# Kernel optimization log

Measured on AMD Instinct MI355X. Metric: run time of the kernel, lower is better.

The kernel has to match this reference:

```python
import jax, jax.numpy as jnp
import numpy as np

E = 20    # number of residue types (rc.restypes)
NB = 2    # num_blocks per AngleHead
NA = 7    # num_angles
C_S = 384
C_H = 128
BS, L = 8, 2048


def setup_inputs() -> dict:
    key = jax.random.key(0)
    ks = jax.random.split(key, 16)
    sc = 0.02
    return {
        "s": jax.random.normal(ks[0], (BS, L, C_S), dtype=jnp.float32),
        "s_init": jax.random.normal(ks[1], (BS, L, C_S), dtype=jnp.float32),
        "aatype": jax.random.randint(ks[2], (BS, L), 0, E, dtype=jnp.int32),
        # stacked per-residue-type AngleHead params
        "Win": jax.random.normal(ks[3], (E, C_S, C_H), dtype=jnp.float32) * sc,
        "b_in": jax.random.normal(ks[4], (E, C_H), dtype=jnp.float32) * sc,
        "Winit": jax.random.normal(ks[5], (E, C_S, C_H), dtype=jnp.float32) * sc,
        "b_init2": jax.random.normal(ks[6], (E, C_H), dtype=jnp.float32) * sc,
        "Wb1": jax.random.normal(ks[7], (E, NB, C_H, C_H), dtype=jnp.float32) * sc,
        "bb1": jax.random.normal(ks[8], (E, NB, C_H), dtype=jnp.float32) * sc,
        "Wb2": jax.random.normal(ks[9], (E, NB, C_H, C_H), dtype=jnp.float32) * sc,
        "bb2": jax.random.normal(ks[10], (E, NB, C_H), dtype=jnp.float32) * sc,
        "Wout": jax.random.normal(ks[11], (E, C_H, NA * 2), dtype=jnp.float32) * sc,
        "b_out": jax.random.normal(ks[12], (E, NA * 2), dtype=jnp.float32) * sc,
    }


def reference(s, s_init, aatype, Win, b_in, Winit, b_init2, Wb1, bb1, Wb2, bb2, Wout, b_out):
    relu = jax.nn.relu
    bs, seq_len, c_s = s.shape
    N = bs * seq_len
    sf = s.reshape(N, c_s)          # [N, c_s]
    si = s_init.reshape(N, c_s)     # [N, c_s]

    # Dense dispatch: run every token through all E per-type heads, then
    # combine with the one-hot routing mask (math identical to the torch
    # gather/scatter loop over residue types).
    h = jnp.einsum('nd,edh->neh', relu(sf), Win) + b_in            # [N,E,H]
    h = h + jnp.einsum('nd,edh->neh', relu(si), Winit) + b_init2   # [N,E,H]

    for b in range(NB):  # ResidualBlock1d: s + W2 @ relu(W1 @ relu(s))
        a = jnp.einsum('neh,ehk->nek', relu(h), Wb1[:, b]) + bb1[:, b]
        a = jnp.einsum('nek,ekh->neh', relu(a), Wb2[:, b]) + bb2[:, b]
        h = h + a

    out = jnp.einsum('neh,eho->neo', relu(h), Wout) + b_out        # [N,E,2*NA]
    sel = jax.nn.one_hot(aatype.reshape(N), E, dtype=out.dtype)    # [N,E]
    ang = jnp.einsum('neo,ne->no', out, sel).reshape(bs, seq_len, NA, 2)

    # F.normalize(dim=-1): x / max(||x||, eps)
    nrm = jnp.maximum(jnp.linalg.norm(ang, axis=-1, keepdims=True), 1e-12)
    return ang / nrm
```

## Files before the change

### kernel.cpp

```cpp
#include <hip/hip_runtime.h>
#include <math.h>

#define E_TYPES 20
#define NBLK 2
#define NANG 7
#define CS 384
#define CH 128
#define N_TOK (8 * 2048)
#define TOK 32
#define TPB 256
#define PREPB 256
#define GRID_M 536
#define PADN 2048

#define CNT_OFF 0
#define PERM_OFF 64
#define WT1_OFF (256 * 1024)
#define WT1_SZ  (20 * 8 * 24 * 2048)
#define WTR_OFF (WT1_OFF + WT1_SZ)

typedef __attribute__((ext_vector_type(8))) short bfrag;
typedef __attribute__((ext_vector_type(4))) float f32x4;

__device__ __forceinline__ void split_bf16(float x, unsigned short& h, unsigned short& l) {
    unsigned int u = __float_as_uint(x);
    unsigned int hb = (u + 0x7FFFu + ((u >> 16) & 1u)) & 0xFFFF0000u;
    h = (unsigned short)(hb >> 16);
    float r = x - __uint_as_float(hb);
    unsigned int v = __float_as_uint(r);
    l = (unsigned short)((v + 0x7FFFu + ((v >> 16) & 1u)) >> 16);
}

__global__ __launch_bounds__(PREPB)
void prep_k(const float* __restrict__ Win, const float* __restrict__ Winit,
            const float* __restrict__ Wb1, const float* __restrict__ Wb2,
            const int* __restrict__ aatype, int* __restrict__ wsI,
            unsigned short* __restrict__ wt)
{
    __shared__ unsigned short tp[4][2][32][134];
    __shared__ int lh[E_TYPES], lcur[E_TYPES];
    int bid = blockIdx.x, t = threadIdx.x;

    if (bid < 64) {
        if (t < E_TYPES) { lh[t] = 0; lcur[t] = 0; }
        __syncthreads();
        for (int i = t; i < bid * 256; i += 256) atomicAdd(&lh[aatype[i]], 1);
        __syncthreads();
        int idx = bid * 256 + t;
        int e = aatype[idx];
        int r = lh[e] + atomicAdd(&lcur[e], 1);
        if (r < PADN) wsI[PERM_OFF + e * PADN + r] = idx;
        if (bid == 63) {
            __syncthreads();
            if (t < E_TYPES) wsI[CNT_OFF + t] = lh[t] + lcur[t];
        }
        return;
    }

    int w = t >> 6, lane = t & 63, lane15 = lane & 15, quad = lane >> 4;
    int wid = (bid - 64) * 4 + w;
    const float* srcbase;
    int phase1, e, kt, m4 = 0;
    if (wid < 480) {
        phase1 = 1;
        e = wid / 24; kt = wid % 24;
        srcbase = (kt < 12) ? Win   + ((size_t)e * CS + kt * 32) * CH
                            : Winit + ((size_t)e * CS + (kt - 12) * 32) * CH;
    } else {
        phase1 = 0;
        int rid = wid - 480;
        e = rid >> 4; m4 = (rid >> 2) & 3; kt = rid & 3;
        const float* W = (m4 & 1) ? Wb2 : Wb1;
        srcbase = W + (((size_t)e * NBLK + (m4 >> 1)) * CH + kt * 32) * CH;
    }

    #pragma unroll 4
    for (int i = 0; i < 16; i++) {
        int idx = i * 64 + lane;
        int row = idx >> 5, c4 = idx & 31;
        float4 v = *(const float4*)(srcbase + (size_t)row * CH + c4 * 4);
        ushort4 hv, lv;
        split_bf16(v.x, hv.x, lv.x);
        split_bf16(v.y, hv.y, lv.y);
        split_bf16(v.z, hv.z, lv.z);
        split_bf16(v.w, hv.w, lv.w);
        *(ushort4*)&tp[w][0][row][c4 * 4] = hv;
        *(ushort4*)&tp[w][1][row][c4 * 4] = lv;
    }
    #pragma unroll
    for (int nt = 0; nt < 8; nt++) {
        bfrag hb, lb;
        #pragma unroll
        for (int j = 0; j < 8; j++) {
            hb[j] = (short)tp[w][0][quad * 8 + j][nt * 16 + lane15];
            lb[j] = (short)tp[w][1][quad * 8 + j][nt * 16 + lane15];
        }
        size_t blk = phase1 ? (size_t)((e * 8 + nt) * 24 + kt)
                            : (size_t)((((e * 4 + m4) * 8) + nt) * 4 + kt);
        unsigned short* dst = wt + (phase1 ? WT1_OFF / 2 : WTR_OFF / 2)
                              + blk * 1024 + lane * 8;
        *(bfrag*)dst = hb;
        *(bfrag*)(dst + 512) = lb;
    }
}

#define MFMA(a, b, c) __builtin_amdgcn_mfma_f32_16x16x32_bf16((a), (b), (c), 0, 0, 0)

#define KSTEP(AH0, AL0, AH1, AL1, B, ACC)                    \
    ACC[0][0] = MFMA(AH0, B[0], ACC[0][0]);                  \
    ACC[0][0] = MFMA(AH0, B[1], ACC[0][0]);                  \
    ACC[0][0] = MFMA(AL0, B[0], ACC[0][0]);                  \
    ACC[0][1] = MFMA(AH0, B[2], ACC[0][1]);                  \
    ACC[0][1] = MFMA(AH0, B[3], ACC[0][1]);                  \
    ACC[0][1] = MFMA(AL0, B[2], ACC[0][1]);                  \
    ACC[1][0] = MFMA(AH1, B[0], ACC[1][0]);                  \
    ACC[1][0] = MFMA(AH1, B[1], ACC[1][0]);                  \
    ACC[1][0] = MFMA(AL1, B[0], ACC[1][0]);                  \
    ACC[1][1] = MFMA(AH1, B[2], ACC[1][1]);                  \
    ACC[1][1] = MFMA(AH1, B[3], ACC[1][1]);                  \
    ACC[1][1] = MFMA(AL1, B[2], ACC[1][1]);

__global__ __launch_bounds__(TPB)
void angle_main(const float* __restrict__ s, const float* __restrict__ si,
                const float* __restrict__ b_in, const float* __restrict__ b_init2,
                const float* __restrict__ bb1, const float* __restrict__ bb2,
                const float* __restrict__ Wout, const float* __restrict__ b_out,
                const int* __restrict__ wsI, const unsigned short* __restrict__ wt,
                float* __restrict__ out)
{
    __shared__ __align__(16) unsigned char smem_raw[32768];
    typedef unsigned short AfragT[2][2][512][8];
    AfragT& Afrag = *reinterpret_cast<AfragT*>(smem_raw);
    float (*Hf)[132] = reinterpret_cast<float(*)[132]>(smem_raw);
    float (*Of)[16]  = reinterpret_cast<float(*)[16]>(smem_raw + 16896);
    __shared__ int ptok[TOK];
    __shared__ int poffs[E_TYPES + 1];

    int t = threadIdx.x;
    if (t <= E_TYPES) {
        int off = 0;
        for (int e = 0; e < t; e++)
            off += (wsI[CNT_OFF + e] + TOK - 1) & ~(TOK - 1);
        poffs[t] = off;
    }
    __syncthreads();

    int bid = blockIdx.x;
    int tile = (bid & 7) * (GRID_M / 8) + (bid >> 3);
    int pos = tile * TOK;
    if (pos >= poffs[E_TYPES]) return;
    int e = 0;
    while (e < E_TYPES - 1 && pos >= poffs[e + 1]) e++;
    int n = wsI[CNT_OFF + e] - (pos - poffs[e]);
    if (n > TOK) n = TOK;
    if (t < TOK)
        ptok[t] = wsI[PERM_OFF + e * PADN + (pos - poffs[e]) + ((t < n) ? t : 0)];

    int w = t >> 6, lane = t & 63, lane15 = lane & 15, quad = lane >> 4;
    int nc0 = (2 * w) * 16 + lane15, nc1 = nc0 + 16;

    __syncthreads();

    const bfrag* wt1 = (const bfrag*)((const char*)wt + WT1_OFF);
    const bfrag* wtr = (const bfrag*)((const char*)wt + WTR_OFF);

    f32x4 acc[2][2];
    {
        float bv0 = b_in[e * CH + nc0] + b_init2[e * CH + nc0];
        float bv1 = b_in[e * CH + nc1] + b_init2[e * CH + nc1];
        #pragma unroll
        for (int mt = 0; mt < 2; mt++) {
            acc[mt][0] = (f32x4){bv0, bv0, bv0, bv0};
            acc[mt][1] = (f32x4){bv1, bv1, bv1, bv1};
        }
    }

    int stok = t >> 3, sc = t & 7;
    const float* rowp_s  = s  + (size_t)ptok[stok] * CS;
    const float* rowp_si = si + (size_t)ptok[stok] * CS;

    float4 pf[2][4];
    #pragma unroll
    for (int q = 0; q < 4; q++)
        pf[0][q] = *(const float4*)(rowp_s + sc * 4 + 32 * q);

    bfrag Bc[4], Bn[4];

    #pragma unroll
    for (int c = 0; c < 6; c++) {
        int buf = c & 1;
        __syncthreads();
        #pragma unroll
        for (int q = 0; q < 4; q++) {
            float4 v = pf[buf][q];
            ushort4 hv, lv;
            split_bf16(fmaxf(v.x, 0.f), hv.x, lv.x);
            split_bf16(fmaxf(v.y, 0.f), hv.y, lv.y);
            split_bf16(fmaxf(v.z, 0.f), hv.z, lv.z);
            split_bf16(fmaxf(v.w, 0.f), hv.w, lv.w);
            int fi = (q * 4 + (sc >> 1)) * 32 + stok;
            *(ushort4*)&Afrag[buf][0][fi][(sc & 1) * 4] = hv;
            *(ushort4*)&Afrag[buf][1][fi][(sc & 1) * 4] = lv;
        }
        __syncthreads();
        if (c + 1 < 6) {
            const float* rp = ((c + 1) < 3 ? rowp_s : rowp_si) + ((c + 1) % 3) * 128;
            #pragma unroll
            for (int q = 0; q < 4; q++)
                pf[(c + 1) & 1][q] = *(const float4*)(rp + sc * 4 + 32 * q);
        }
        {
            size_t b0 = ((size_t)(e * 8 + 2 * w) * 24 + c * 4) * 128;
            size_t b1 = ((size_t)(e * 8 + 2 * w + 1) * 24 + c * 4) * 128;
            Bc[0] = wt1[b0 + lane]; Bc[1] = wt1[b0 + 64 + lane];
            Bc[2] = wt1[b1 + lane]; Bc[3] = wt1[b1 + 64 + lane];
        }
        #pragma unroll
        for (int ks = 0; ks < 4; ks++) {
            if (ks < 3) {
                int kb = c * 4 + ks + 1;
                size_t b0 = ((size_t)(e * 8 + 2 * w) * 24 + kb) * 128;
                size_t b1 = ((size_t)(e * 8 + 2 * w + 1) * 24 + kb) * 128;
                Bn[0] = wt1[b0 + lane]; Bn[1] = wt1[b0 + 64 + lane];
                Bn[2] = wt1[b1 + lane]; Bn[3] = wt1[b1 + 64 + lane];
            }
            int fib = (ks * 4 + quad) * 32;
            bfrag ah0 = *(const bfrag*)&Afrag[buf][0][fib + lane15][0];
            bfrag ah1 = *(const bfrag*)&Afrag[buf][0][fib + 16 + lane15][0];
            bfrag al0 = *(const bfrag*)&Afrag[buf][1][fib + lane15][0];
            bfrag al1 = *(const bfrag*)&Afrag[buf][1][fib + 16 + lane15][0];
            KSTEP(ah0, al0, ah1, al1, Bc, acc)
            #pragma unroll
            for (int z = 0; z < 4; z++) Bc[z] = Bn[z];
        }
    }

    f32x4 a2[2][2];
    #pragma unroll
    for (int b = 0; b < NBLK; b++) {
        #pragma unroll
        for (int stage = 0; stage < 2; stage++) {
            int g = 2 * b + stage;
            __syncthreads();
            #pragma unroll
            for (int mt = 0; mt < 2; mt++)
                #pragma unroll
                for (int nl = 0; nl < 2; nl++) {
                    f32x4 v = (stage == 0) ? acc[mt][nl] : a2[mt][nl];
                    int nn = (2 * w + nl) * 16 + lane15;
                    int fib = ((nn >> 5) * 4 + ((nn >> 3) & 3)) * 32;
                    int j = nn & 7;
                    #pragma unroll
                    for (int r = 0; r < 4; r++) {
                        int m = mt * 16 + quad * 4 + r;
                        unsigned short hh, ll;
                        split_bf16(fmaxf(v[r], 0.f), hh, ll);
                        Afrag[0][0][fib + m][j] = hh;
                        Afrag[0][1][fib + m][j] = ll;
                    }
                }
            __syncthreads();

            const float* bias = (stage == 0) ? bb1 : bb2;
            f32x4 an[2][2];
            {
                float bv0 = bias[(e * NBLK + b) * CH + nc0];
                float bv1 = bias[(e * NBLK + b) * CH + nc1];
                #pragma unroll
                for (int mt = 0; mt < 2; mt++) {
                    an[mt][0] = (f32x4){bv0, bv0, bv0, bv0};
                    an[mt][1] = (f32x4){bv1, bv1, bv1, bv1};
                }
            }
            {
                size_t b0 = ((size_t)((e * 4 + g) * 8 + 2 * w) * 4) * 128;
                size_t b1 = ((size_t)((e * 4 + g) * 8 + 2 * w + 1) * 4) * 128;
                Bc[0] = wtr[b0 + lane]; Bc[1] = wtr[b0 + 64 + lane];
                Bc[2] = wtr[b1 + lane]; Bc[3] = wtr[b1 + 64 + lane];
            }
            #pragma unroll
            for (int ks = 0; ks < 4; ks++) {
                if (ks < 3) {
                    size_t b0 = ((size_t)((e * 4 + g) * 8 + 2 * w) * 4 + ks + 1) * 128;
                    size_t b1 = ((size_t)((e * 4 + g) * 8 + 2 * w + 1) * 4 + ks + 1) * 128;
                    Bn[0] = wtr[b0 + lane]; Bn[1] = wtr[b0 + 64 + lane];
                    Bn[2] = wtr[b1 + lane]; Bn[3] = wtr[b1 + 64 + lane];
                }
                int fib = (ks * 4 + quad) * 32;
                bfrag ah0 = *(const bfrag*)&Afrag[0][0][fib + lane15][0];
                bfrag ah1 = *(const bfrag*)&Afrag[0][0][fib + 16 + lane15][0];
                bfrag al0 = *(const bfrag*)&Afrag[0][1][fib + lane15][0];
                bfrag al1 = *(const bfrag*)&Afrag[0][1][fib + 16 + lane15][0];
                KSTEP(ah0, al0, ah1, al1, Bc, an)
                #pragma unroll
                for (int z = 0; z < 4; z++) Bc[z] = Bn[z];
            }
            if (stage == 0) {
                #pragma unroll
                for (int mt = 0; mt < 2; mt++)
                    #pragma unroll
                    for (int nl = 0; nl < 2; nl++) a2[mt][nl] = an[mt][nl];
            } else {
                #pragma unroll
                for (int mt = 0; mt < 2; mt++)
                    #pragma unroll
                    for (int nl = 0; nl < 2; nl++) acc[mt][nl] += an[mt][nl];
            }
        }
    }

    __syncthreads();
    #pragma unroll
    for (int mt = 0; mt < 2; mt++)
        #pragma unroll
        for (int nl = 0; nl < 2; nl++) {
            f32x4 v = acc[mt][nl];
            int nn = (2 * w + nl) * 16 + lane15;
            #pragma unroll
            for (int r = 0; r < 4; r++)
                Hf[mt * 16 + quad * 4 + r][nn] = fmaxf(v[r], 0.f);
        }
    __syncthreads();

    const float* WoutE = Wout + (size_t)e * CH * (NANG * 2);
    const float* boutE = b_out + (size_t)e * (NANG * 2);
    for (int idx = t; idx < n * (NANG * 2); idx += TPB) {
        int i = idx / (NANG * 2);
        int o = idx % (NANG * 2);
        float v = boutE[o];
        #pragma unroll 4
        for (int k = 0; k < CH; k++)
            v = fmaf(Hf[i][k], WoutE[(size_t)k * (NANG * 2) + o], v);
        Of[i][o] = v;
    }
    __syncthreads();

    for (int idx = t; idx < n * NANG; idx += TPB) {
        int i = idx / NANG;
        int a = idx % NANG;
        float x = Of[i][2 * a];
        float y = Of[i][2 * a + 1];
        float nr = fmaxf(sqrtf(x * x + y * y), 1e-12f);
        size_t base = (size_t)ptok[i] * (NANG * 2) + 2 * a;
        out[base]     = x / nr;
        out[base + 1] = y / nr;
    }
}

extern "C" void kernel_launch(void* const* d_in, const int* in_sizes, int n_in,
                              void* d_out, int out_size, void* d_ws, size_t ws_size,
                              hipStream_t stream) {
    const float* s       = (const float*)d_in[0];
    const float* s_init  = (const float*)d_in[1];
    const int*   aatype  = (const int*)d_in[2];
    const float* Win     = (const float*)d_in[3];
    const float* b_in    = (const float*)d_in[4];
    const float* Winit   = (const float*)d_in[5];
    const float* b_init2 = (const float*)d_in[6];
    const float* Wb1     = (const float*)d_in[7];
    const float* bb1     = (const float*)d_in[8];
    const float* Wb2     = (const float*)d_in[9];
    const float* bb2     = (const float*)d_in[10];
    const float* Wout    = (const float*)d_in[11];
    const float* b_out   = (const float*)d_in[12];
    int* wsI = (int*)d_ws;
    unsigned short* wt = (unsigned short*)d_ws;
    float* out = (float*)d_out;

    hipLaunchKernelGGL(prep_k, dim3(64 + 200), dim3(PREPB), 0, stream,
                       Win, Winit, Wb1, Wb2, aatype, wsI, wt);
    hipLaunchKernelGGL(angle_main, dim3(GRID_M), dim3(TPB), 0, stream,
                       s, s_init, b_in, b_init2, bb1, bb2, Wout, b_out,
                       wsI, wt, out);
}
```

Before: 168.2 us.

## Stage weight fragments into LDS via global_load_lds and swizzle A tiles

Weight B fragments are now copied from global memory straight into per-wave LDS buffers with global_load_lds (16-byte DMA) instead of being loaded into registers with software double buffering. The A fragment tile is shrunk to 64-wide K chunks (12 steps instead of 6), and an XOR swizzle is applied to its LDS layout to cut bank conflicts. The aim is to lower VGPR pressure and global-load latency stalls. In exchange the kernel uses more LDS per block (48KB), which can reduce occupancy, and it synchronises more often per K chunk.

```diff
diff --git a/kernel.cpp b/kernel.cpp
--- a/kernel.cpp
+++ b/kernel.cpp
@@ -21,6 +21,13 @@
 
 typedef __attribute__((ext_vector_type(8))) short bfrag;
 typedef __attribute__((ext_vector_type(4))) float f32x4;
+typedef unsigned int u32;
+typedef __attribute__((address_space(1))) const u32 gu32;
+typedef __attribute__((address_space(3))) u32 lu32;
+
+__device__ __forceinline__ void dma16(const void* g, void* l) {
+    __builtin_amdgcn_global_load_lds((gu32*)g, (lu32*)l, 16, 0, 0);
+}
 
 __device__ __forceinline__ void split_bf16(float x, unsigned short& h, unsigned short& l) {
     unsigned int u = __float_as_uint(x);
@@ -29,6 +36,10 @@
     float r = x - __uint_as_float(hb);
     unsigned int v = __float_as_uint(r);
     l = (unsigned short)((v + 0x7FFFu + ((v >> 16) & 1u)) >> 16);
+}
+
+__device__ __forceinline__ int SWZ(int K, int m) {
+    return K * 32 + (m ^ ((4 * K) & 31));
 }
 
 __global__ __launch_bounds__(PREPB)
@@ -106,19 +117,21 @@
 
 #define MFMA(a, b, c) __builtin_amdgcn_mfma_f32_16x16x32_bf16((a), (b), (c), 0, 0, 0)
 
-#define KSTEP(AH0, AL0, AH1, AL1, B, ACC)                    \
-    ACC[0][0] = MFMA(AH0, B[0], ACC[0][0]);                  \
-    ACC[0][0] = MFMA(AH0, B[1], ACC[0][0]);                  \
-    ACC[0][0] = MFMA(AL0, B[0], ACC[0][0]);                  \
-    ACC[0][1] = MFMA(AH0, B[2], ACC[0][1]);                  \
-    ACC[0][1] = MFMA(AH0, B[3], ACC[0][1]);                  \
-    ACC[0][1] = MFMA(AL0, B[2], ACC[0][1]);                  \
-    ACC[1][0] = MFMA(AH1, B[0], ACC[1][0]);                  \
-    ACC[1][0] = MFMA(AH1, B[1], ACC[1][0]);                  \
-    ACC[1][0] = MFMA(AL1, B[0], ACC[1][0]);                  \
-    ACC[1][1] = MFMA(AH1, B[2], ACC[1][1]);                  \
-    ACC[1][1] = MFMA(AH1, B[3], ACC[1][1]);                  \
-    ACC[1][1] = MFMA(AL1, B[2], ACC[1][1]);
+#define KSTEP(AH0, AL0, AH1, AL1, BH0, BL0, BH1, BL1, ACC)   \
+    ACC[0][0] = MFMA(AH0, BH0, ACC[0][0]);                   \
+    ACC[0][0] = MFMA(AH0, BL0, ACC[0][0]);                   \
+    ACC[0][0] = MFMA(AL0, BH0, ACC[0][0]);                   \
+    ACC[0][1] = MFMA(AH0, BH1, ACC[0][1]);                   \
+    ACC[0][1] = MFMA(AH0, BL1, ACC[0][1]);                   \
+    ACC[0][1] = MFMA(AL0, BH1, ACC[0][1]);                   \
+    ACC[1][0] = MFMA(AH1, BH0, ACC[1][0]);                   \
+    ACC[1][0] = MFMA(AH1, BL0, ACC[1][0]);                   \
+    ACC[1][0] = MFMA(AL1, BH0, ACC[1][0]);                   \
+    ACC[1][1] = MFMA(AH1, BH1, ACC[1][1]);                   \
+    ACC[1][1] = MFMA(AH1, BL1, ACC[1][1]);                   \
+    ACC[1][1] = MFMA(AL1, BH1, ACC[1][1]);
+
+#define AIDX(buf, p, fi) ((((buf) * 2 + (p)) * 256 + (fi)) * 8)
 
 __global__ __launch_bounds__(TPB)
 void angle_main(const float* __restrict__ s, const float* __restrict__ si,
@@ -128,11 +141,11 @@
                 const int* __restrict__ wsI, const unsigned short* __restrict__ wt,
                 float* __restrict__ out)
 {
-    __shared__ __align__(16) unsigned char smem_raw[32768];
-    typedef unsigned short AfragT[2][2][512][8];
-    AfragT& Afrag = *reinterpret_cast<AfragT*>(smem_raw);
-    float (*Hf)[132] = reinterpret_cast<float(*)[132]>(smem_raw);
-    float (*Of)[16]  = reinterpret_cast<float(*)[16]>(smem_raw + 16896);
+    __shared__ __align__(16) unsigned char smem_raw[49152];
+    unsigned short* A = (unsigned short*)smem_raw;
+    unsigned char*  Bb = smem_raw + 16384;
+    float (*Hf)[132] = reinterpret_cast<float(*)[132]>(smem_raw + 16384);
+    float (*Of)[16]  = reinterpret_cast<float(*)[16]>(smem_raw + 16384 + 16896);
     __shared__ int ptok[TOK];
     __shared__ int poffs[E_TYPES + 1];
 
@@ -158,11 +171,9 @@
 
     int w = t >> 6, lane = t & 63, lane15 = lane & 15, quad = lane >> 4;
     int nc0 = (2 * w) * 16 + lane15, nc1 = nc0 + 16;
+    unsigned char* Bw = Bb + w * 8192;
 
     __syncthreads();
-
-    const bfrag* wt1 = (const bfrag*)((const char*)wt + WT1_OFF);
-    const bfrag* wtr = (const bfrag*)((const char*)wt + WTR_OFF);
 
     f32x4 acc[2][2];
     {
@@ -178,60 +189,56 @@
     int stok = t >> 3, sc = t & 7;
     const float* rowp_s  = s  + (size_t)ptok[stok] * CS;
     const float* rowp_si = si + (size_t)ptok[stok] * CS;
-
-    float4 pf[2][4];
-    #pragma unroll
-    for (int q = 0; q < 4; q++)
-        pf[0][q] = *(const float4*)(rowp_s + sc * 4 + 32 * q);
-
-    bfrag Bc[4], Bn[4];
-
-    #pragma unroll
-    for (int c = 0; c < 6; c++) {
+    int fiA = SWZ(sc, stok);
+
+    float4 pf[2][2];
+    pf[0][0] = *(const float4*)(rowp_s + sc * 8);
+    pf[0][1] = *(const float4*)(rowp_s + sc * 8 + 4);
+
+    const char* wt1b = (const char*)wt + WT1_OFF;
+    const char* wtrb = (const char*)wt + WTR_OFF;
+
+    for (int c = 0; c < 12; c++) {
         int buf = c & 1;
-        __syncthreads();
-        #pragma unroll
-        for (int q = 0; q < 4; q++) {
+        #pragma unroll
+        for (int q = 0; q < 2; q++) {
             float4 v = pf[buf][q];
             ushort4 hv, lv;
             split_bf16(fmaxf(v.x, 0.f), hv.x, lv.x);
             split_bf16(fmaxf(v.y, 0.f), hv.y, lv.y);
             split_bf16(fmaxf(v.z, 0.f), hv.z, lv.z);
             split_bf16(fmaxf(v.w, 0.f), hv.w, lv.w);
-            int fi = (q * 4 + (sc >> 1)) * 32 + stok;
-            *(ushort4*)&Afrag[buf][0][fi][(sc & 1) * 4] = hv;
-            *(ushort4*)&Afrag[buf][1][fi][(sc & 1) * 4] = lv;
-        }
+            *(ushort4*)&A[AIDX(buf, 0, fiA) + 4 * q] = hv;
+            *(ushort4*)&A[AIDX(buf, 1, fiA) + 4 * q] = lv;
+        }
+        #pragma unroll
+        for (int ksl = 0; ksl < 2; ksl++)
+            #pragma unroll
+            for (int nl = 0; nl < 2; nl++) {
+                size_t blk = (size_t)((e * 8 + 2 * w + nl) * 24 + (c * 2 + ksl));
+                const char* g = wt1b + blk * 2048 + lane * 16;
+                dma16(g,        Bw + (ksl * 4 + nl * 2 + 0) * 1024);
+                dma16(g + 1024, Bw + (ksl * 4 + nl * 2 + 1) * 1024);
+            }
         __syncthreads();
-        if (c + 1 < 6) {
-            const float* rp = ((c + 1) < 3 ? rowp_s : rowp_si) + ((c + 1) % 3) * 128;
-            #pragma unroll
-            for (int q = 0; q < 4; q++)
-                pf[(c + 1) & 1][q] = *(const float4*)(rp + sc * 4 + 32 * q);
-        }
-        {
-            size_t b0 = ((size_t)(e * 8 + 2 * w) * 24 + c * 4) * 128;
-            size_t b1 = ((size_t)(e * 8 + 2 * w + 1) * 24 + c * 4) * 128;
-            Bc[0] = wt1[b0 + lane]; Bc[1] = wt1[b0 + 64 + lane];
-            Bc[2] = wt1[b1 + lane]; Bc[3] = wt1[b1 + 64 + lane];
-        }
-        #pragma unroll
-        for (int ks = 0; ks < 4; ks++) {
-            if (ks < 3) {
-                int kb = c * 4 + ks + 1;
-                size_t b0 = ((size_t)(e * 8 + 2 * w) * 24 + kb) * 128;
-                size_t b1 = ((size_t)(e * 8 + 2 * w + 1) * 24 + kb) * 128;
-                Bn[0] = wt1[b0 + lane]; Bn[1] = wt1[b0 + 64 + lane];
-                Bn[2] = wt1[b1 + lane]; Bn[3] = wt1[b1 + 64 + lane];
-            }
-            int fib = (ks * 4 + quad) * 32;
-            bfrag ah0 = *(const bfrag*)&Afrag[buf][0][fib + lane15][0];
-            bfrag ah1 = *(const bfrag*)&Afrag[buf][0][fib + 16 + lane15][0];
-            bfrag al0 = *(const bfrag*)&Afrag[buf][1][fib + lane15][0];
-            bfrag al1 = *(const bfrag*)&Afrag[buf][1][fib + 16 + lane15][0];
-            KSTEP(ah0, al0, ah1, al1, Bc, acc)
-            #pragma unroll
-            for (int z = 0; z < 4; z++) Bc[z] = Bn[z];
+        if (c + 1 < 12) {
+            const float* rp = ((c + 1) < 6 ? rowp_s : rowp_si) + ((c + 1) % 6) * 64 + sc * 8;
+            pf[buf ^ 1][0] = *(const float4*)(rp);
+            pf[buf ^ 1][1] = *(const float4*)(rp + 4);
+        }
+        #pragma unroll
+        for (int ksl = 0; ksl < 2; ksl++) {
+            int K = ksl * 4 + quad;
+            bfrag ah0 = *(const bfrag*)&A[AIDX(buf, 0, SWZ(K, lane15))];
+            bfrag ah1 = *(const bfrag*)&A[AIDX(buf, 0, SWZ(K, 16 + lane15))];
+            bfrag al0 = *(const bfrag*)&A[AIDX(buf, 1, SWZ(K, lane15))];
+            bfrag al1 = *(const bfrag*)&A[AIDX(buf, 1, SWZ(K, 16 + lane15))];
+            const unsigned char* bs = Bw + ksl * 4096 + lane * 16;
+            bfrag bh0 = *(const bfrag*)(bs);
+            bfrag bl0 = *(const bfrag*)(bs + 1024);
+            bfrag bh1 = *(const bfrag*)(bs + 2048);
+            bfrag bl1 = *(const bfrag*)(bs + 3072);
+            KSTEP(ah0, al0, ah1, al1, bh0, bl0, bh1, bl1, acc)
         }
     }
 
@@ -247,17 +254,28 @@
                 #pragma unroll
                 for (int nl = 0; nl < 2; nl++) {
                     f32x4 v = (stage == 0) ? acc[mt][nl] : a2[mt][nl];
-                    int nn = (2 * w + nl) * 16 + lane15;
-                    int fib = ((nn >> 5) * 4 + ((nn >> 3) & 3)) * 32;
+                    int nn = 32 * w + 16 * nl + lane15;
+                    int ab = w >> 1;
+                    int K = (nn >> 3) & 7;
                     int j = nn & 7;
                     #pragma unroll
                     for (int r = 0; r < 4; r++) {
                         int m = mt * 16 + quad * 4 + r;
+                        int fi = SWZ(K, m);
                         unsigned short hh, ll;
                         split_bf16(fmaxf(v[r], 0.f), hh, ll);
-                        Afrag[0][0][fib + m][j] = hh;
-                        Afrag[0][1][fib + m][j] = ll;
+                        A[AIDX(ab, 0, fi) + j] = hh;
+                        A[AIDX(ab, 1, fi) + j] = ll;
                     }
+                }
+            #pragma unroll
+            for (int ksl = 0; ksl < 2; ksl++)
+                #pragma unroll
+                for (int nl = 0; nl < 2; nl++) {
+                    size_t blk = (size_t)(((e * 4 + g) * 8 + 2 * w + nl) * 4 + ksl);
+                    const char* gp = wtrb + blk * 2048 + lane * 16;
+                    dma16(gp,        Bw + (ksl * 4 + nl * 2 + 0) * 1024);
+                    dma16(gp + 1024, Bw + (ksl * 4 + nl * 2 + 1) * 1024);
                 }
             __syncthreads();
 
@@ -272,28 +290,43 @@
                     an[mt][1] = (f32x4){bv1, bv1, bv1, bv1};
                 }
             }
-            {
-                size_t b0 = ((size_t)((e * 4 + g) * 8 + 2 * w) * 4) * 128;
-                size_t b1 = ((size_t)((e * 4 + g) * 8 + 2 * w + 1) * 4) * 128;
-                Bc[0] = wtr[b0 + lane]; Bc[1] = wtr[b0 + 64 + lane];
-                Bc[2] = wtr[b1 + lane]; Bc[3] = wtr[b1 + 64 + lane];
+            #pragma unroll
+            for (int ksl = 0; ksl < 2; ksl++) {
+                int K = ksl * 4 + quad;
+                bfrag ah0 = *(const bfrag*)&A[AIDX(0, 0, SWZ(K, lane15))];
+                bfrag ah1 = *(const bfrag*)&A[AIDX(0, 0, SWZ(K, 16 + lane15))];
+                bfrag al0 = *(const bfrag*)&A[AIDX(0, 1, SWZ(K, lane15))];
+                bfrag al1 = *(const bfrag*)&A[AIDX(0, 1, SWZ(K, 16 + lane15))];
+                const unsigned char* bs = Bw + ksl * 4096 + lane * 16;
+                bfrag bh0 = *(const bfrag*)(bs);
+                bfrag bl0 = *(const bfrag*)(bs + 1024);
+                bfrag bh1 = *(const bfrag*)(bs + 2048);
+                bfrag bl1 = *(const bfrag*)(bs + 3072);
+                KSTEP(ah0, al0, ah1, al1, bh0, bl0, bh1, bl1, an)
             }
             #pragma unroll
-            for (int ks = 0; ks < 4; ks++) {
-                if (ks < 3) {
-                    size_t b0 = ((size_t)((e * 4 + g) * 8 + 2 * w) * 4 + ks + 1) * 128;
-                    size_t b1 = ((size_t)((e * 4 + g) * 8 + 2 * w + 1) * 4 + ks + 1) * 128;
-                    Bn[0] = wtr[b0 + lane]; Bn[1] = wtr[b0 + 64 + lane];
-                    Bn[2] = wtr[b1 + lane]; Bn[3] = wtr[b1 + 64 + lane];
+            for (int ksl = 0; ksl < 2; ksl++)
+                #pragma unroll
+                for (int nl = 0; nl < 2; nl++) {
+                    size_t blk = (size_t)(((e * 4 + g) * 8 + 2 * w + nl) * 4 + 2 + ksl);
+                    const char* gp = wtrb + blk * 2048 + lane * 16;
+                    dma16(gp,        Bw + (ksl * 4 + nl * 2 + 0) * 1024);
+                    dma16(gp + 1024, Bw + (ksl * 4 + nl * 2 + 1) * 1024);
                 }
-                int fib = (ks * 4 + quad) * 32;
-                bfrag ah0 = *(const bfrag*)&Afrag[0][0][fib + lane15][0];
-                bfrag ah1 = *(const bfrag*)&Afrag[0][0][fib + 16 + lane15][0];
-                bfrag al0 = *(const bfrag*)&Afrag[0][1][fib + lane15][0];
-                bfrag al1 = *(const bfrag*)&Afrag[0][1][fib + 16 + lane15][0];
-                KSTEP(ah0, al0, ah1, al1, Bc, an)
-                #pragma unroll
-                for (int z = 0; z < 4; z++) Bc[z] = Bn[z];
+            __syncthreads();
+            #pragma unroll
+            for (int ksl = 0; ksl < 2; ksl++) {
+                int K = ksl * 4 + quad;
+                bfrag ah0 = *(const bfrag*)&A[AIDX(1, 0, SWZ(K, lane15))];
+                bfrag ah1 = *(const bfrag*)&A[AIDX(1, 0, SWZ(K, 16 + lane15))];
+                bfrag al0 = *(const bfrag*)&A[AIDX(1, 1, SWZ(K, lane15))];
+                bfrag al1 = *(const bfrag*)&A[AIDX(1, 1, SWZ(K, 16 + lane15))];
+                const unsigned char* bs = Bw + ksl * 4096 + lane * 16;
+                bfrag bh0 = *(const bfrag*)(bs);
+                bfrag bl0 = *(const bfrag*)(bs + 1024);
+                bfrag bh1 = *(const bfrag*)(bs + 2048);
+                bfrag bl1 = *(const bfrag*)(bs + 3072);
+                KSTEP(ah0, al0, ah1, al1, bh0, bl0, bh1, bl1, an)
             }
             if (stage == 0) {
                 #pragma unroll
@@ -315,7 +348,7 @@
         #pragma unroll
         for (int nl = 0; nl < 2; nl++) {
             f32x4 v = acc[mt][nl];
-            int nn = (2 * w + nl) * 16 + lane15;
+            int nn = 32 * w + 16 * nl + lane15;
             #pragma unroll
             for (int r = 0; r < 4; r++)
                 Hf[mt * 16 + quad * 4 + r][nn] = fmaxf(v[r], 0.f);
```

New measurement: 171.9 us. 2.2% more time.
